# Kernel optimization log

Hardware: AMD Instinct MI355X
Metric: run time of the kernel (lower is better)

The kernel has to match this reference:

```python
import jax, jax.numpy as jnp
import numpy as np

B, S, E, H = 32, 1024, 256, 256


def setup_inputs() -> dict:
    key = jax.random.key(0)
    ks = jax.random.split(key, 12)
    sc = 0.02
    return {
        "encoder_inputs": jax.random.normal(ks[0], (B, S, E), jnp.float32),
        "decoder_input": jax.random.normal(ks[1], (B, E), jnp.float32),
        "h0": jax.random.normal(ks[2], (B, H), jnp.float32),
        "c0": jax.random.normal(ks[3], (B, H), jnp.float32),
        "context": jax.random.normal(ks[4], (B, S, H), jnp.float32),
        "W_ih": jax.random.normal(ks[5], (E, 4 * H), jnp.float32) * sc,
        "b_ih": jnp.zeros((4 * H,), jnp.float32),
        "W_hh": jax.random.normal(ks[6], (H, 4 * H), jnp.float32) * sc,
        "b_hh": jnp.zeros((4 * H,), jnp.float32),
        "W_out": jax.random.normal(ks[7], (2 * H, H), jnp.float32) * sc,
        "b_out": jnp.zeros((H,), jnp.float32),
        "Wa_in": jax.random.normal(ks[8], (H, H), jnp.float32) * sc,
        "ba_in": jnp.zeros((H,), jnp.float32),
        "Wa_ctx": jax.random.normal(ks[9], (H, H), jnp.float32) * sc,
        "ba_ctx": jnp.zeros((H,), jnp.float32),
        "v": jax.random.normal(ks[10], (H,), jnp.float32) * sc,
    }


def reference(encoder_inputs, decoder_input, h0, c0, context,
              W_ih, b_ih, W_hh, b_hh, W_out, b_out,
              Wa_in, ba_in, Wa_ctx, ba_ctx, v):
    bsz, seq_len, _ = encoder_inputs.shape
    # Project context once (Attention.context_linear); reused every step.
    ctx_proj = jnp.einsum('bsh,hk->bsk', context, Wa_ctx) + ba_ctx  # [B,S,H]

    def step(carry, _):
        x, h, c, mask = carry  # mask: 1.0 = still available
        gates = x @ W_ih + b_ih + h @ W_hh + b_hh  # [B,4H]
        i, f, g, o = jnp.split(gates, 4, axis=1)   # chunk order: input, forget, cell, out
        c_t = jax.nn.sigmoid(f) * c + jax.nn.sigmoid(i) * jnp.tanh(g)
        h_t = jax.nn.sigmoid(o) * jnp.tanh(c_t)
        # Additive (Bahdanau-style) attention
        inp = h_t @ Wa_in + ba_in                                  # [B,H]
        scores = jnp.einsum('h,bsh->bs', v, jnp.tanh(inp[:, None, :] + ctx_proj))
        scores = jnp.where(mask > 0, scores, -jnp.inf)             # mask selected positions
        alpha = jax.nn.softmax(scores, axis=-1)                    # [B,S]
        attn_hidden = jnp.einsum('bs,bsh->bh', alpha, ctx_proj)    # weighted projected context
        h_out = jnp.tanh(jnp.concatenate([attn_hidden, h_t], axis=1) @ W_out + b_out)
        # Pointer selection + mask/input update
        idx = jnp.argmax(alpha * mask, axis=-1)                    # [B]
        one_ptr = jax.nn.one_hot(idx, seq_len, dtype=mask.dtype)   # [B,S]
        new_mask = mask * (1.0 - one_ptr)
        x_next = jnp.einsum('bs,bse->be', one_ptr, encoder_inputs)
        return (x_next, h_out, c_t, new_mask), (alpha, idx)

    mask0 = jnp.ones((bsz, seq_len), jnp.float32)
    _, (alphas, ptrs) = jax.lax.scan(step, (decoder_input, h0, c0, mask0), None, length=seq_len)
    outputs = jnp.transpose(alphas, (1, 0, 2))  # [B,S,S] attention distribution per step
    pointers = jnp.transpose(ptrs, (1, 0))      # [B,S] selected indices
    return outputs, pointers
```

## Files before the change

### kernel.cpp

```cpp
#include <hip/hip_runtime.h>
#include <math.h>

#define BB 32
#define SSS 1024
#define EE 256
#define HHH 256
#define TEAM 8
#define CHUNK 128
#define NTHR 512
#define CPAD 129
#define THETA 3e-5f
#define MAXCAND 8

#define NEG_INF (-__builtin_huge_valf())

__device__ __forceinline__ double sigd(double x) {
  return 1.0 / (1.0 + exp(-x));
}

__device__ __forceinline__ float fast_tanhf(float x) {
  float e = __expf(2.0f * x);
  return 1.0f - 2.0f * __builtin_amdgcn_rcpf(1.0f + e);
}

__device__ __forceinline__ void gstore(float* p, float v) {
  __hip_atomic_store(p, v, __ATOMIC_RELAXED, __HIP_MEMORY_SCOPE_AGENT);
}
__device__ __forceinline__ float gload(const float* p) {
  return __hip_atomic_load(p, __ATOMIC_RELAXED, __HIP_MEMORY_SCOPE_AGENT);
}
__device__ __forceinline__ void gstored(double* p, double v) {
  __hip_atomic_store(p, v, __ATOMIC_RELAXED, __HIP_MEMORY_SCOPE_AGENT);
}
__device__ __forceinline__ double gloadd(const double* p) {
  return __hip_atomic_load(p, __ATOMIC_RELAXED, __HIP_MEMORY_SCOPE_AGENT);
}

__device__ __forceinline__ void bar_arrive(int* cnt) {
  __syncthreads();
  if (threadIdx.x == 0)
    __hip_atomic_fetch_add(cnt, 1, __ATOMIC_RELEASE, __HIP_MEMORY_SCOPE_AGENT);
}
__device__ __forceinline__ void bar_wait(int* cnt, int target) {
  if (threadIdx.x == 0) {
    while (__hip_atomic_load(cnt, __ATOMIC_RELAXED, __HIP_MEMORY_SCOPE_AGENT) < target) {}
  }
  __syncthreads();
}
__device__ __forceinline__ void team_bar(int* cnt, int target) {
  bar_arrive(cnt);
  bar_wait(cnt, target);
}

__global__ __launch_bounds__(NTHR, 1) void ptrnet(
    const float* __restrict__ enc, const float* __restrict__ dec0,
    const float* __restrict__ h0, const float* __restrict__ c0,
    const float* __restrict__ context,
    const float* __restrict__ W_ih, const float* __restrict__ b_ih,
    const float* __restrict__ W_hh, const float* __restrict__ b_hh,
    const float* __restrict__ W_out, const float* __restrict__ b_out,
    const float* __restrict__ Wa_in, const float* __restrict__ ba_in,
    const float* __restrict__ Wa_ctx, const float* __restrict__ ba_ctx,
    const float* __restrict__ v,
    float* __restrict__ out,
    int* __restrict__ barp,
    float* __restrict__ hbuf, float* __restrict__ htbuf,
    float* __restrict__ pinp, float* __restrict__ stats,
    float* __restrict__ accb, double* __restrict__ refws)
{
  __shared__ __align__(16) float cpT[HHH * CPAD];
  __shared__ double dsc[256];
  __shared__ __align__(8) float ivp[HHH * 2];
  __shared__ double inp_d[HHH];
  __shared__ float attn_s[HHH];
  __shared__ float ht_s[HHH];
  __shared__ __align__(16) float hx_s[HHH];
  __shared__ __align__(16) float x_s[EE];
  __shared__ float scratch[NTHR];
  __shared__ float bg_s[128];
  __shared__ float bain_s[HHH];
  __shared__ float v_s[HHH];
  __shared__ float score_s[CHUNK];
  __shared__ float w_s[CHUNK];
  __shared__ float alive_s[CHUNK];
  __shared__ float bo_s[32];
  __shared__ float htl_s[32];
  __shared__ float scale8_s[TEAM];
  __shared__ float mg_sh, linv_sh, cutoff_sh;
  __shared__ int idx_sh, rf_sh, ncand_sh;
  __shared__ int cand_s[MAXCAND];

  const int tid = threadIdx.x;
  const int b = blockIdx.x & 31;
  const int m = blockIdx.x >> 5;
  int* cnt = barp + b * 32;

  {
    float* raw = cpT;
    const float* ctxp = context + ((size_t)b * SSS + (size_t)m * CHUNK) * HHH;
    for (int i = tid; i < CHUNK * HHH; i += NTHR) raw[i] = ctxp[i];
    __syncthreads();
    const int cc = tid & 255;
    const int rgc = tid >> 8;
    double acc[2][32];
    double bc = (double)ba_ctx[cc];
    for (int half = 0; half < 2; ++half) {
#pragma unroll
      for (int k = 0; k < 32; ++k) acc[half][k] = 0.0;
      for (int h = 0; h < HHH; ++h) {
        double w = (double)Wa_ctx[h * HHH + cc];
        const float* base = &raw[(rgc * 64 + half * 32) * HHH + h];
#pragma unroll
        for (int k = 0; k < 32; ++k) acc[half][k] = fma((double)base[k * HHH], w, acc[half][k]);
      }
    }
    __syncthreads();
#pragma unroll
    for (int half = 0; half < 2; ++half)
#pragma unroll
      for (int k = 0; k < 32; ++k) {
        int row = rgc * 64 + half * 32 + k;
        cpT[cc * CPAD + row] = (float)(acc[half][k] + bc);
      }
  }

  const int q = tid & 127, rg = tid >> 7;
  const int gcol = ((q >> 5) * 256) + m * 32 + (q & 31);
  float w_ih_r[64], w_hh_r[64];
#pragma unroll
  for (int k = 0; k < 64; ++k) {
    w_ih_r[k] = W_ih[(size_t)(rg * 64 + k) * 1024 + gcol];
    w_hh_r[k] = W_hh[(size_t)(rg * 64 + k) * 1024 + gcol];
  }
  const int hp = tid & 255, rh = tid >> 8;
  float w_ain_r[16];
#pragma unroll
  for (int k = 0; k < 16; ++k)
    w_ain_r[k] = Wa_in[(size_t)(m * 32 + rh * 16 + k) * HHH + hp];
  const int c2 = tid & 31, rgo = tid >> 5;
  float w_out_r[32];
#pragma unroll
  for (int k = 0; k < 32; ++k)
    w_out_r[k] = W_out[(size_t)(rgo * 32 + k) * HHH + m * 32 + c2];

  if (tid < 128) {
    int j = ((tid >> 5) * 256) + m * 32 + (tid & 31);
    bg_s[tid] = b_ih[j] + b_hh[j];
    alive_s[tid] = 1.0f;
  }
  if (tid < 256) { bain_s[tid] = ba_in[tid]; v_s[tid] = v[tid]; }
  if (tid < 32)  bo_s[tid] = b_out[m * 32 + tid];
  double c_reg = (tid < 32) ? (double)c0[b * HHH + m * 32 + tid] : 0.0;
  __syncthreads();

  int bart = 0;

  for (int t = 0; t < SSS; ++t) {
    if (tid < 256) {
      x_s[tid] = (t == 0) ? dec0[b * EE + tid]
                          : enc[((size_t)b * SSS + (size_t)idx_sh) * EE + tid];
    }
    if (t > 0) bar_wait(cnt, bart);
    if (tid < 256) hx_s[tid] = (t == 0) ? h0[b * HHH + tid] : gload(&hbuf[b * HHH + tid]);
    __syncthreads();
    {
      float ax0 = 0.0f, ax1 = 0.0f, ah0 = 0.0f, ah1 = 0.0f;
      const float4* x4 = reinterpret_cast<const float4*>(&x_s[rg * 64]);
      const float4* h4 = reinterpret_cast<const float4*>(&hx_s[rg * 64]);
#pragma unroll
      for (int k = 0; k < 16; k += 2) {
        float4 xv0 = x4[k], xv1 = x4[k + 1];
        ax0 = fmaf(w_ih_r[4 * k + 0], xv0.x, ax0);
        ax0 = fmaf(w_ih_r[4 * k + 1], xv0.y, ax0);
        ax0 = fmaf(w_ih_r[4 * k + 2], xv0.z, ax0);
        ax0 = fmaf(w_ih_r[4 * k + 3], xv0.w, ax0);
        ax1 = fmaf(w_ih_r[4 * k + 4], xv1.x, ax1);
        ax1 = fmaf(w_ih_r[4 * k + 5], xv1.y, ax1);
        ax1 = fmaf(w_ih_r[4 * k + 6], xv1.z, ax1);
        ax1 = fmaf(w_ih_r[4 * k + 7], xv1.w, ax1);
      }
#pragma unroll
      for (int k = 0; k < 16; k += 2) {
        float4 hv0 = h4[k], hv1 = h4[k + 1];
        ah0 = fmaf(w_hh_r[4 * k + 0], hv0.x, ah0);
        ah0 = fmaf(w_hh_r[4 * k + 1], hv0.y, ah0);
        ah0 = fmaf(w_hh_r[4 * k + 2], hv0.z, ah0);
        ah0 = fmaf(w_hh_r[4 * k + 3], hv0.w, ah0);
        ah1 = fmaf(w_hh_r[4 * k + 4], hv1.x, ah1);
        ah1 = fmaf(w_hh_r[4 * k + 5], hv1.y, ah1);
        ah1 = fmaf(w_hh_r[4 * k + 6], hv1.z, ah1);
        ah1 = fmaf(w_hh_r[4 * k + 7], hv1.w, ah1);
      }
      scratch[tid] = (ax0 + ah0) + (ax1 + ah1);
    }
    __syncthreads();
    if (tid < 64) {
      const int g0 = tid;
      const int g1 = tid + 64;
      float s0 = scratch[g0] + scratch[128 + g0] + scratch[256 + g0] + scratch[384 + g0] + bg_s[g0];
      float s1 = scratch[g1] + scratch[128 + g1] + scratch[256 + g1] + scratch[384 + g1] + bg_s[g1];
      double act0 = sigd((double)s0);
      double act1 = (tid < 32) ? tanh((double)s1) : sigd((double)s1);
      double f_ = __shfl_xor(act0, 32);
      double o_ = __shfl_xor(act1, 32);
      if (tid < 32) {
        double cn = f_ * c_reg + act0 * act1;
        double ht = o_ * tanh(cn);
        c_reg = cn;
        float htf = (float)ht;
        htl_s[tid] = htf;
        gstore(&htbuf[b * HHH + m * 32 + tid], htf);
      }
    }
    __syncthreads();
    {
      float p = 0.0f;
#pragma unroll
      for (int k = 0; k < 16; ++k) p = fmaf(w_ain_r[k], htl_s[rh * 16 + k], p);
      scratch[rh * 256 + hp] = p;
    }
    __syncthreads();
    if (tid < 256) gstore(&pinp[((b * TEAM) + m) * HHH + tid], scratch[tid] + scratch[256 + tid]);
    bart += TEAM; team_bar(cnt, bart);

    if (tid < 256) {
      double sd = (double)bain_s[tid];
#pragma unroll
      for (int w = 0; w < TEAM; ++w) sd += (double)gload(&pinp[((b * TEAM) + w) * HHH + tid]);
      inp_d[tid] = sd;
      ivp[2 * tid] = (float)sd; ivp[2 * tid + 1] = v_s[tid];
    }
    __syncthreads();
    {
      const int s = tid & 127, qq = tid >> 7;
      const float* cpc = &cpT[(qq * 64) * CPAD + s];
      const float2* iv = reinterpret_cast<const float2*>(&ivp[2 * qq * 64]);
      float a0 = 0.0f, a1 = 0.0f, a2 = 0.0f, a3 = 0.0f;
#pragma unroll 4
      for (int j = 0; j < 64; j += 4) {
        float2 iv0 = iv[j], iv1 = iv[j + 1], iv2 = iv[j + 2], iv3 = iv[j + 3];
        a0 = fmaf(iv0.y, fast_tanhf(iv0.x + cpc[(j + 0) * CPAD]), a0);
        a1 = fmaf(iv1.y, fast_tanhf(iv1.x + cpc[(j + 1) * CPAD]), a1);
        a2 = fmaf(iv2.y, fast_tanhf(iv2.x + cpc[(j + 2) * CPAD]), a2);
        a3 = fmaf(iv3.y, fast_tanhf(iv3.x + cpc[(j + 3) * CPAD]), a3);
      }
      scratch[tid] = (a0 + a1) + (a2 + a3);
    }
    __syncthreads();
    if (tid < 128)
      score_s[tid] = scratch[tid] + scratch[128 + tid] + scratch[256 + tid] + scratch[384 + tid];
    __syncthreads();
    if (tid < 64) {
      float sa = (alive_s[tid] > 0.0f) ? score_s[tid] : NEG_INF;
      float sb = (alive_s[tid + 64] > 0.0f) ? score_s[tid + 64] : NEG_INF;
      float v1, v2; int i1;
      if (sb > sa) { v1 = sb; i1 = tid + 64; v2 = sa; }
      else         { v1 = sa; i1 = tid;      v2 = sb; }
#pragma unroll
      for (int d = 1; d < 64; d <<= 1) {
        float ov1 = __shfl_xor(v1, d); int oi1 = __shfl_xor(i1, d);
        float ov2 = __shfl_xor(v2, d);
        if (ov1 > v1 || (ov1 == v1 && oi1 < i1)) {
          v2 = fmaxf(v1, ov2); v1 = ov1; i1 = oi1;
        } else {
          v2 = fmaxf(v2, ov1);
        }
      }
      float w0 = (alive_s[tid] > 0.0f) ? __expf(score_s[tid] - v1) : 0.0f;
      float w1 = (alive_s[tid + 64] > 0.0f) ? __expf(score_s[tid + 64] - v1) : 0.0f;
      w_s[tid] = w0; w_s[tid + 64] = w1;
      float l = w0 + w1;
#pragma unroll
      for (int d = 1; d < 64; d <<= 1) l += __shfl_xor(l, d);
      if (tid == 0) {
        float* st = &stats[((b * TEAM) + m) * 4];
        gstore(&st[0], v1);
        gstore(&st[1], l);
        gstore(&st[2], __int_as_float((v1 == NEG_INF) ? 0x7fffffff : (m * CHUNK + i1)));
        gstore(&st[3], v2);
      }
    }
    __syncthreads();
    {
      const int h = tid & 255, sh = tid >> 8;
      const float* cpr = &cpT[h * CPAD + sh * 64];
      const float* wr = &w_s[sh * 64];
      float a0 = 0.0f, a1 = 0.0f, a2 = 0.0f, a3 = 0.0f;
#pragma unroll 4
      for (int j = 0; j < 64; j += 4) {
        a0 = fmaf(wr[j + 0], cpr[j + 0], a0);
        a1 = fmaf(wr[j + 1], cpr[j + 1], a1);
        a2 = fmaf(wr[j + 2], cpr[j + 2], a2);
        a3 = fmaf(wr[j + 3], cpr[j + 3], a3);
      }
      scratch[sh * 256 + h] = (a0 + a1) + (a2 + a3);
    }
    __syncthreads();
    if (tid < 256) gstore(&accb[((b * TEAM) + m) * HHH + tid], scratch[tid] + scratch[256 + tid]);
    bart += TEAM; team_bar(cnt, bart);

    float accp[TEAM]; float htp = 0.0f;
    if (tid < 256) {
#pragma unroll
      for (int w = 0; w < TEAM; ++w) accp[w] = gload(&accb[((b * TEAM) + w) * HHH + tid]);
      htp = gload(&htbuf[b * HHH + tid]);
    }
    if (tid < 32)
      scratch[tid] = gload(&stats[((b * TEAM) + (tid >> 2)) * 4 + (tid & 3)]);
    __syncthreads();
    if (tid == 0) {
      float g1 = NEG_INF, g2 = NEG_INF; int gi = 0x7fffffff;
      float mcv[TEAM], lcv[TEAM];
#pragma unroll
      for (int w = 0; w < TEAM; ++w) {
        mcv[w] = scratch[w * 4 + 0]; lcv[w] = scratch[w * 4 + 1];
        int biv = __float_as_int(scratch[w * 4 + 2]); float v2v = scratch[w * 4 + 3];
        if (lcv[w] > 0.0f) {
          if (mcv[w] > g1 || (mcv[w] == g1 && biv < gi)) {
            g2 = fmaxf(g1, v2v); g1 = mcv[w]; gi = biv;
          } else {
            g2 = fmaxf(g2, mcv[w]);
          }
        }
      }
      float sw[TEAM]; float lg = 0.0f;
#pragma unroll
      for (int w = 0; w < TEAM; ++w) {
        sw[w] = (lcv[w] > 0.0f) ? __expf(mcv[w] - g1) : 0.0f;
        lg += lcv[w] * sw[w];
      }
      float linv = __builtin_amdgcn_rcpf(lg);
#pragma unroll
      for (int w = 0; w < TEAM; ++w) scale8_s[w] = sw[w] * linv;
      mg_sh = g1; linv_sh = linv; idx_sh = gi;
      rf_sh = (g2 > g1 - THETA) ? 1 : 0;
      cutoff_sh = g1 - THETA;
    }
    __syncthreads();

    if (tid < 128) {
      float sc_ = score_s[tid];
      float al = (alive_s[tid] > 0.0f) ? __expf(sc_ - mg_sh) * linv_sh : 0.0f;
      __builtin_nontemporal_store(al,
          &out[(size_t)b * (SSS * SSS) + (size_t)t * SSS + m * CHUNK + tid]);
    }

    if (rf_sh) {
      if (tid == 0) {
        int nc = 0;
        for (int s2 = 0; s2 < CHUNK; ++s2)
          if (alive_s[s2] > 0.0f && score_s[s2] > cutoff_sh && nc < MAXCAND)
            cand_s[nc++] = s2;
        ncand_sh = nc;
      }
      __syncthreads();
      const int nc = ncand_sh;
      for (int ci = 0; ci < nc; ++ci) {
        const int slot = cand_s[ci];
        if (tid < 256) {
          const float* crow = context + ((size_t)b * SSS + (size_t)(m * CHUNK + slot)) * HHH;
          double acc = (double)ba_ctx[tid];
          for (int h2 = 0; h2 < HHH; ++h2)
            acc = fma((double)crow[h2], (double)Wa_ctx[h2 * HHH + tid], acc);
          double arg = inp_d[tid] + acc;
          dsc[tid] = (double)v_s[tid] * tanh(arg);
        }
        __syncthreads();
        if (tid < 64) {
          double se = dsc[tid] + dsc[tid + 64] + dsc[tid + 128] + dsc[tid + 192];
#pragma unroll
          for (int d = 1; d < 64; d <<= 1) se += __shfl_xor(se, d);
          if (tid == 0) {
            double* rw = &refws[(((size_t)b * TEAM) + m) * (1 + 2 * MAXCAND)];
            gstored(&rw[1 + 2 * ci], (double)(m * CHUNK + slot));
            gstored(&rw[2 + 2 * ci], se);
          }
        }
        __syncthreads();
      }
      if (tid == 0)
        gstored(&refws[(((size_t)b * TEAM) + m) * (1 + 2 * MAXCAND)], (double)nc);
      bart += TEAM; team_bar(cnt, bart);
      if (tid == 0) {
        double bs = -1.0e300; int bi2 = 0x7fffffff;
#pragma unroll
        for (int w = 0; w < TEAM; ++w) {
          const double* rw = &refws[(((size_t)b * TEAM) + w) * (1 + 2 * MAXCAND)];
          int wn = (int)gloadd(&rw[0]);
          for (int j2 = 0; j2 < wn; ++j2) {
            int ii = (int)gloadd(&rw[1 + 2 * j2]); double sv = gloadd(&rw[2 + 2 * j2]);
            if (sv > bs || (sv == bs && ii < bi2)) { bs = sv; bi2 = ii; }
          }
        }
        idx_sh = bi2;
      }
      __syncthreads();
    }

    if (tid < 256) {
      float a0 = 0.0f, a1 = 0.0f;
#pragma unroll
      for (int w = 0; w < TEAM; w += 2) {
        a0 = fmaf(accp[w], scale8_s[w], a0);
        a1 = fmaf(accp[w + 1], scale8_s[w + 1], a1);
      }
      attn_s[tid] = a0 + a1;
      ht_s[tid] = htp;
    }
    __syncthreads();
    {
      const float* srcp = (rgo < 8) ? &attn_s[rgo * 32] : &ht_s[(rgo - 8) * 32];
      float h0a = 0.0f, h1a = 0.0f;
#pragma unroll
      for (int k = 0; k < 32; k += 2) {
        h0a = fmaf(w_out_r[k], srcp[k], h0a);
        h1a = fmaf(w_out_r[k + 1], srcp[k + 1], h1a);
      }
      scratch[rgo * 32 + c2] = h0a + h1a;
    }
    __syncthreads();
    if (tid < 32) {
      float s = bo_s[tid];
#pragma unroll
      for (int j = 0; j < 16; ++j) s += scratch[j * 32 + tid];
      gstore(&hbuf[b * HHH + m * 32 + tid], tanhf(s));
    }
    if (m == 0 && tid == 0)
      __builtin_nontemporal_store((float)idx_sh,
          &out[(size_t)BB * SSS * SSS + (size_t)b * SSS + t]);
    if (tid == 0 && (idx_sh >> 7) == m) alive_s[idx_sh & 127] = 0.0f;
    bart += TEAM; bar_arrive(cnt);
  }
}

extern "C" void kernel_launch(void* const* d_in, const int* in_sizes, int n_in,
                              void* d_out, int out_size, void* d_ws, size_t ws_size,
                              hipStream_t stream) {
  (void)in_sizes; (void)n_in; (void)out_size; (void)ws_size;
  const float* enc     = (const float*)d_in[0];
  const float* dec0    = (const float*)d_in[1];
  const float* h0      = (const float*)d_in[2];
  const float* c0      = (const float*)d_in[3];
  const float* context = (const float*)d_in[4];
  const float* W_ih    = (const float*)d_in[5];
  const float* b_ih    = (const float*)d_in[6];
  const float* W_hh    = (const float*)d_in[7];
  const float* b_hh    = (const float*)d_in[8];
  const float* W_out   = (const float*)d_in[9];
  const float* b_out   = (const float*)d_in[10];
  const float* Wa_in   = (const float*)d_in[11];
  const float* ba_in   = (const float*)d_in[12];
  const float* Wa_ctx  = (const float*)d_in[13];
  const float* ba_ctx  = (const float*)d_in[14];
  const float* v       = (const float*)d_in[15];

  char* wsb   = (char*)d_ws;
  int*   barp  = (int*)wsb;
  float* hbuf  = (float*)(wsb + 4096);
  float* htbuf = hbuf + 32 * 256;
  float* pinp  = htbuf + 32 * 256;
  float* stats = pinp + 32 * 8 * 256;
  float* accb  = stats + 32 * 8 * 4;
  double* refws = (double*)(accb + 32 * 8 * 256);

  hipMemsetAsync(d_ws, 0, 4096, stream);
  hipLaunchKernelGGL(ptrnet, dim3(256), dim3(NTHR), 0, stream,
                     enc, dec0, h0, c0, context,
                     W_ih, b_ih, W_hh, b_hh, W_out, b_out,
                     Wa_in, ba_in, Wa_ctx, ba_ctx, v,
                     (float*)d_out, barp, hbuf, htbuf, pinp, stats, accb, refws);
}
```

Measured before the change: 26.41 ms.

## Merge split barrier into full team barrier and spread gate activations across 128 threads

Replaces the split arrive/wait barrier at the end of each step, which let the next step's x load overlap the wait, with a single full team barrier. The gate activations are now computed by 128 threads writing to shared memory instead of 64 threads using shuffles, with the cell state kept in shared memory. Launch bounds now allow 2 blocks per CU. This drops the overlap of the encoder-row load with the barrier wait in exchange for simpler sync and more parallel transcendental evaluation, at the cost of one extra __syncthreads per step.

```diff
diff --git a/kernel.cpp b/kernel.cpp
--- a/kernel.cpp
+++ b/kernel.cpp
@@ -36,23 +36,16 @@
   return __hip_atomic_load(p, __ATOMIC_RELAXED, __HIP_MEMORY_SCOPE_AGENT);
 }
 
-__device__ __forceinline__ void bar_arrive(int* cnt) {
+__device__ __forceinline__ void team_bar(int* cnt, int target) {
   __syncthreads();
-  if (threadIdx.x == 0)
+  if (threadIdx.x == 0) {
     __hip_atomic_fetch_add(cnt, 1, __ATOMIC_RELEASE, __HIP_MEMORY_SCOPE_AGENT);
-}
-__device__ __forceinline__ void bar_wait(int* cnt, int target) {
-  if (threadIdx.x == 0) {
     while (__hip_atomic_load(cnt, __ATOMIC_RELAXED, __HIP_MEMORY_SCOPE_AGENT) < target) {}
   }
   __syncthreads();
 }
-__device__ __forceinline__ void team_bar(int* cnt, int target) {
-  bar_arrive(cnt);
-  bar_wait(cnt, target);
-}
-
-__global__ __launch_bounds__(NTHR, 1) void ptrnet(
+
+__global__ __launch_bounds__(NTHR, 2) void ptrnet(
     const float* __restrict__ enc, const float* __restrict__ dec0,
     const float* __restrict__ h0, const float* __restrict__ c0,
     const float* __restrict__ context,
@@ -72,6 +65,7 @@
   __shared__ double dsc[256];
   __shared__ __align__(8) float ivp[HHH * 2];
   __shared__ double inp_d[HHH];
+  __shared__ double gact[128];
   __shared__ float attn_s[HHH];
   __shared__ float ht_s[HHH];
   __shared__ __align__(16) float hx_s[HHH];
@@ -85,6 +79,7 @@
   __shared__ float alive_s[CHUNK];
   __shared__ float bo_s[32];
   __shared__ float htl_s[32];
+  __shared__ double c_d[32];
   __shared__ float scale8_s[TEAM];
   __shared__ float mg_sh, linv_sh, cutoff_sh;
   __shared__ int idx_sh, rf_sh, ncand_sh;
@@ -149,19 +144,20 @@
     alive_s[tid] = 1.0f;
   }
   if (tid < 256) { bain_s[tid] = ba_in[tid]; v_s[tid] = v[tid]; }
-  if (tid < 32)  bo_s[tid] = b_out[m * 32 + tid];
-  double c_reg = (tid < 32) ? (double)c0[b * HHH + m * 32 + tid] : 0.0;
+  if (tid < 32)  { bo_s[tid] = b_out[m * 32 + tid]; c_d[tid] = (double)c0[b * HHH + m * 32 + tid]; }
   __syncthreads();
 
   int bart = 0;
 
   for (int t = 0; t < SSS; ++t) {
     if (tid < 256) {
-      x_s[tid] = (t == 0) ? dec0[b * EE + tid]
-                          : enc[((size_t)b * SSS + (size_t)idx_sh) * EE + tid];
-    }
-    if (t > 0) bar_wait(cnt, bart);
-    if (tid < 256) hx_s[tid] = (t == 0) ? h0[b * HHH + tid] : gload(&hbuf[b * HHH + tid]);
+      if (t == 0) { x_s[tid] = dec0[b * EE + tid]; hx_s[tid] = h0[b * HHH + tid]; }
+      else {
+        int ix = idx_sh;
+        x_s[tid] = enc[((size_t)b * SSS + ix) * EE + tid];
+        hx_s[tid] = gload(&hbuf[b * HHH + tid]);
+      }
+    }
     __syncthreads();
     {
       float ax0 = 0.0f, ax1 = 0.0f, ah0 = 0.0f, ah1 = 0.0f;
@@ -194,23 +190,19 @@
       scratch[tid] = (ax0 + ah0) + (ax1 + ah1);
     }
     __syncthreads();
-    if (tid < 64) {
-      const int g0 = tid;
-      const int g1 = tid + 64;
-      float s0 = scratch[g0] + scratch[128 + g0] + scratch[256 + g0] + scratch[384 + g0] + bg_s[g0];
-      float s1 = scratch[g1] + scratch[128 + g1] + scratch[256 + g1] + scratch[384 + g1] + bg_s[g1];
-      double act0 = sigd((double)s0);
-      double act1 = (tid < 32) ? tanh((double)s1) : sigd((double)s1);
-      double f_ = __shfl_xor(act0, 32);
-      double o_ = __shfl_xor(act1, 32);
-      if (tid < 32) {
-        double cn = f_ * c_reg + act0 * act1;
-        double ht = o_ * tanh(cn);
-        c_reg = cn;
-        float htf = (float)ht;
-        htl_s[tid] = htf;
-        gstore(&htbuf[b * HHH + m * 32 + tid], htf);
-      }
+    if (tid < 128) {
+      float gsv = scratch[tid] + scratch[128 + tid] + scratch[256 + tid] + scratch[384 + tid] + bg_s[tid];
+      double gd = (double)gsv;
+      gact[tid] = (tid >= 64 && tid < 96) ? tanh(gd) : sigd(gd);
+    }
+    __syncthreads();
+    if (tid < 32) {
+      double cn = gact[32 + tid] * c_d[tid] + gact[tid] * gact[64 + tid];
+      double ht = gact[96 + tid] * tanh(cn);
+      c_d[tid] = cn;
+      float htf = (float)ht;
+      htl_s[tid] = htf;
+      gstore(&htbuf[b * HHH + m * 32 + tid], htf);
     }
     __syncthreads();
     {
@@ -429,7 +421,7 @@
       __builtin_nontemporal_store((float)idx_sh,
           &out[(size_t)BB * SSS * SSS + (size_t)b * SSS + t]);
     if (tid == 0 && (idx_sh >> 7) == m) alive_s[idx_sh & 127] = 0.0f;
-    bart += TEAM; bar_arrive(cnt);
+    bart += TEAM; team_bar(cnt, bart);
   }
 }
 
```

Result: no change. 26.24 ms (-0.7%).
